# Kernel optimization log

Measured on AMD Instinct MI355X. Metric: run time of the kernel, lower is better.

The kernel has to match this reference:

```python
import jax, jax.numpy as jnp
import numpy as np
from jax import lax

NH = 4          # num_head
DIM = 512       # attention dim
VDIM = 512      # v_dim
QDIM = 1024     # q_dim
KS = 100        # loc_kernel_size -> conv width 2*KS+1
KN = 100        # loc_kernel_num
TEMP = 0.5      # temperature
BS, TS = 8, 2048


def setup_inputs() -> dict:
    key = jax.random.key(0)
    ks = jax.random.split(key, 12)
    s = 0.05
    return {
        "dec_state": jax.random.normal(ks[0], (BS, QDIM), jnp.float32),
        "enc_feat": jax.random.normal(ks[1], (BS, TS, VDIM), jnp.float32),
        "enc_len": jax.random.randint(ks[2], (BS,), TS // 2, TS + 1).astype(jnp.int32),
        "Wq": jax.random.normal(ks[3], (NH * DIM, QDIM), jnp.float32) * s,
        "bq": jnp.zeros((NH * DIM,), jnp.float32),
        "Wk": jax.random.normal(ks[4], (NH * DIM, VDIM), jnp.float32) * s,
        "bk": jnp.zeros((NH * DIM,), jnp.float32),
        "Wv": jax.random.normal(ks[5], (NH * VDIM, VDIM), jnp.float32) * s,
        "bv": jnp.zeros((NH * VDIM,), jnp.float32),
        "loc_conv_w": jax.random.normal(ks[6], (KN, NH, 2 * KS + 1), jnp.float32) * s,
        "loc_proj_w": jax.random.normal(ks[7], (DIM, KN), jnp.float32) * s,
        "gen_w": jax.random.normal(ks[8], (1, DIM), jnp.float32) * s,
        "gen_b": jnp.zeros((1,), jnp.float32),
        "merge_w": jax.random.normal(ks[9], (VDIM, NH * VDIM), jnp.float32) * s,
        "merge_b": jnp.zeros((VDIM,), jnp.float32),
    }


def reference(dec_state, enc_feat, enc_len, Wq, bq, Wk, bk, Wv, bv,
              loc_conv_w, loc_proj_w, gen_w, gen_b, merge_w, merge_b):
    bs, ts, _ = enc_feat.shape
    # query: [bs, nh, dim]
    query = jnp.tanh(dec_state @ Wq.T + bq).reshape(bs, NH, DIM)
    # key/value: [bs, nh, ts, dim]/[bs, nh, ts, v_dim]
    key = jnp.tanh(enc_feat @ Wk.T + bk).reshape(bs, ts, NH, DIM).transpose(0, 2, 1, 3)
    value = jnp.tanh(enc_feat @ Wv.T + bv).reshape(bs, ts, NH, VDIM).transpose(0, 2, 1, 3)
    # mask & initial (uniform-over-valid) previous attention
    pos = jnp.arange(ts)
    pad_mask = pos[None, :] >= enc_len[:, None]                      # [bs, ts] True = padded
    prev = jnp.where(pad_mask, 0.0, 1.0 / enc_len[:, None].astype(jnp.float32))  # [bs, ts]
    prev_att = jnp.broadcast_to(prev[:, None, :], (bs, NH, ts))      # [bs, nh, ts]
    # location features: Conv1d(nh -> kn, width 2*KS+1, pad KS, no bias)
    conv = lax.conv_general_dilated(prev_att, loc_conv_w, (1,), [(KS, KS)],
                                    dimension_numbers=("NCH", "OIH", "NCH"))  # [bs, kn, ts]
    loc = jnp.tanh(jnp.einsum("bkt,dk->btd", conv, loc_proj_w))      # [bs, ts, dim]
    # additive energy: gen_energy(tanh(k + q + loc))
    e = jnp.tanh(key + query[:, :, None, :] + loc[:, None, :, :])    # [bs, nh, ts, dim]
    energy = jnp.einsum("bhtd,d->bht", e, gen_w[0]) + gen_b[0]
    energy = energy / TEMP
    energy = jnp.where(pad_mask[:, None, :], -jnp.inf, energy)
    attn = jax.nn.softmax(energy, axis=-1)                           # [bs, nh, ts]
    ctx = jnp.einsum("bht,bhtv->bhv", attn, value).reshape(bs, NH * VDIM)
    context = ctx @ merge_w.T + merge_b                              # [bs, v_dim]
    return attn, context
```

## Files before the change

### kernel.cpp

```cpp
#include <hip/hip_runtime.h>
#include <math.h>

#define NH 4
#define DIM 512
#define VDIM 512
#define QDIM 1024
#define KS 100
#define KN 100
#define TEMPERATURE 0.5f
#define BS 8
#define TS 2048
#define NHD (NH * DIM)

#define WS_QUERY  0
#define WS_QTAB   16384
#define WS_ENERGY 119808
#define WS_CTX    185344
#define WS_P      201728
#define WS_F32_END 221928

typedef __bf16 bf16x8 __attribute__((ext_vector_type(8)));
typedef __bf16 bf16x4 __attribute__((ext_vector_type(4)));
typedef float  f32x4  __attribute__((ext_vector_type(4)));

#define AS1(p) ((const __attribute__((address_space(1))) void*)(p))
#define AS3(p) ((__attribute__((address_space(3))) void*)(p))

__device__ __forceinline__ float fast_tanh(float x) {
    float xc = fminf(fmaxf(x, -9.0f), 9.0f);
    float e = __expf(2.0f * xc);
    return __fdividef(e - 1.0f, e + 1.0f);
}

#define NE4 (BS * TS * VDIM / 4)
#define NW4 (NHD * VDIM / 4)
#define NCVT ((NE4 + 2 * NW4) / 256)
#define NQRY (BS * NHD / 4)
__global__ void k_precvt(const float* __restrict__ enc, const float* __restrict__ Wk,
                         const float* __restrict__ Wv, __bf16* __restrict__ enc_bf,
                         __bf16* __restrict__ wk_bf, __bf16* __restrict__ wv_bf,
                         const float* __restrict__ dec, const float* __restrict__ Wq,
                         const float* __restrict__ bq, float* __restrict__ query,
                         const float* __restrict__ convw, float* __restrict__ P) {
    if (blockIdx.x < NCVT) {
        int i = blockIdx.x * blockDim.x + threadIdx.x;
        const float* src; __bf16* dst; int k;
        if (i < NE4)            { src = enc; dst = enc_bf; k = i; }
        else if (i < NE4 + NW4) { src = Wk;  dst = wk_bf;  k = i - NE4; }
        else                    { src = Wv;  dst = wv_bf;  k = i - NE4 - NW4; }
        float4 v = ((const float4*)src)[k];
        bf16x4 o;
        o[0] = (__bf16)v.x; o[1] = (__bf16)v.y; o[2] = (__bf16)v.z; o[3] = (__bf16)v.w;
        ((bf16x4*)dst)[k] = o;
    } else if (blockIdx.x < NCVT + NQRY) {
        int q = blockIdx.x - NCVT;
        int w = q * 4 + (threadIdx.x >> 6);
        int lane = threadIdx.x & 63;
        int b = w >> 11;
        int o = w & 2047;
        const float* dr = dec + b * QDIM;
        const float* wr = Wq + o * QDIM;
        float s = 0.f;
        #pragma unroll
        for (int i = 0; i < QDIM / 64; ++i)
            s = fmaf(dr[lane + 64 * i], wr[lane + 64 * i], s);
        #pragma unroll
        for (int off = 32; off > 0; off >>= 1) s += __shfl_down(s, off);
        if (lane == 0) query[b * NHD + o] = tanhf(s + bq[o]);
    } else {
        int k = threadIdx.x;
        if (k < KN) {
            const float* wr = convw + k * (NH * (2 * KS + 1));
            float acc = 0.f;
            P[k] = 0.f;
            for (int dt = 0; dt < 2 * KS + 1; ++dt) {
                acc += wr[dt] + wr[201 + dt] + wr[402 + dt] + wr[603 + dt];
                P[(dt + 1) * KN + k] = acc;
            }
        }
    }
}

__global__ void k_qtab(const float* __restrict__ P, const float* __restrict__ projw,
                       float* __restrict__ Qtab) {
    int j = blockIdx.x;
    __shared__ float Pc[KN];
    int tid = threadIdx.x;
    if (tid < KN) Pc[tid] = P[j * KN + tid];
    __syncthreads();
    const float* pr = projw + tid * KN;
    float s = 0.f;
    #pragma unroll 4
    for (int k = 0; k < KN; ++k) s = fmaf(pr[k], Pc[k], s);
    Qtab[j * DIM + tid] = s;
}

#define GEMM1(Bptr)                                                               \
    const int bid = blockIdx.x;                                                    \
    const int b   = bid >> 8;                                                      \
    const int t0  = ((bid >> 4) & 15) << 7;                                        \
    const int n0  = ((((bid >> 3) & 1) << 3) | (bid & 7)) << 7;                    \
    const int len = enc_len[b];                                                    \
    if (t0 >= len) return;                                                         \
    const int tid = threadIdx.x;                                                   \
    const int w = tid >> 6, lane = tid & 63;                                       \
    const int wy = w >> 2, wx = w & 3;                                             \
    const int col = lane & 15, quad = lane >> 4;                                   \
    __shared__ __bf16 Ash[2 * 4096];                                               \
    __shared__ __bf16 Bsh[2 * 4096];                                               \
    f32x4 acc[4][2];                                                               \
    _Pragma("unroll")                                                              \
    for (int i = 0; i < 4; ++i)                                                    \
        _Pragma("unroll")                                                          \
        for (int j = 0; j < 2; ++j) acc[i][j] = (f32x4)0.f;                        \
    const __bf16* Abase = enc_bf + ((size_t)b * TS + t0) * VDIM;                   \
    const int sm = tid >> 2;                                                       \
    const int sj = (tid & 3) ^ (sm & 3) ^ ((sm >> 2) & 3);                         \
    const __bf16* gpA = Abase + (size_t)sm * VDIM + sj * 8;                        \
    const __bf16* gpB = (Bptr) + ((size_t)n0 + sm) * VDIM + sj * 8;                \
    const int cfr = quad ^ (col & 3) ^ ((col >> 2) & 3);                           \
    const char* pA = (const char*)Ash + (((wy * 64 + col) * 4 + cfr) << 4);        \
    const char* pB = (const char*)Bsh + (((wx * 32 + col) * 4 + cfr) << 4);        \
    __builtin_amdgcn_global_load_lds(AS1(gpA), AS3(Ash + w * 512), 16, 0, 0);      \
    __builtin_amdgcn_global_load_lds(AS1(gpB), AS3(Bsh + w * 512), 16, 0, 0);      \
    gpA += 32; gpB += 32;                                                          \
    for (int kk = 0; kk < 16; ++kk) {                                              \
        __syncthreads();                                                           \
        if (kk < 15) {                                                             \
            int nb_ = ((kk + 1) & 1) * 4096;                                       \
            __builtin_amdgcn_global_load_lds(AS1(gpA), AS3(Ash + nb_ + w * 512), 16, 0, 0); \
            __builtin_amdgcn_global_load_lds(AS1(gpB), AS3(Bsh + nb_ + w * 512), 16, 0, 0); \
            gpA += 32; gpB += 32;                                                  \
        }                                                                          \
        const int bo = (kk & 1) * 8192;                                            \
        bf16x8 af[4], bfr[2];                                                      \
        _Pragma("unroll")                                                          \
        for (int i = 0; i < 4; ++i) af[i] = *(const bf16x8*)(pA + bo + i * 1024);  \
        _Pragma("unroll")                                                          \
        for (int j = 0; j < 2; ++j) bfr[j] = *(const bf16x8*)(pB + bo + j * 1024); \
        _Pragma("unroll")                                                          \
        for (int i = 0; i < 4; ++i)                                                \
            _Pragma("unroll")                                                      \
            for (int j = 0; j < 2; ++j)                                            \
                acc[i][j] = __builtin_amdgcn_mfma_f32_16x16x32_bf16(               \
                    af[i], bfr[j], acc[i][j], 0, 0, 0);                            \
    }                                                                              \
    __syncthreads();

__global__ __launch_bounds__(512, 4) void k_energy(
    const __bf16* __restrict__ enc_bf, const __bf16* __restrict__ wk_bf,
    const float* __restrict__ bk, const float* __restrict__ gen_w,
    const int* __restrict__ enc_len, const float* __restrict__ query,
    const float* __restrict__ Qtab, float* __restrict__ energy) {
    GEMM1(wk_bf)

    const int h = n0 >> 9;
    const float inv_len = 1.0f / (float)len;
    float qv[2], gw[2], bkv[2], lI[2];
    int dj[2];
    #pragma unroll
    for (int j = 0; j < 2; ++j) {
        int n = n0 + wx * 32 + j * 16 + col;
        dj[j] = n & (DIM - 1);
        qv[j] = query[b * NHD + n];
        gw[j] = gen_w[dj[j]];
        bkv[j] = bk[n];
        lI[j] = fast_tanh((Qtab[(2 * KS + 1) * DIM + dj[j]] - Qtab[dj[j]]) * inv_len);
    }
    float* red = (float*)Ash;
    #pragma unroll
    for (int i = 0; i < 4; ++i) {
        #pragma unroll
        for (int r = 0; r < 4; ++r) {
            int tl = wy * 64 + i * 16 + quad * 4 + r;
            int t = t0 + tl;
            float l[2];
            if (t >= KS && t < len - KS) {
                #pragma unroll
                for (int j = 0; j < 2; ++j) l[j] = lI[j];
            } else {
                int lo = KS - t; if (lo < 0) lo = 0;
                int hi = KS - t + len - 1; if (hi > 2 * KS) hi = 2 * KS;
                bool has = (hi >= lo);
                #pragma unroll
                for (int j = 0; j < 2; ++j) {
                    float cv = has
                        ? (Qtab[(hi + 1) * DIM + dj[j]] - Qtab[lo * DIM + dj[j]]) * inv_len
                        : 0.f;
                    l[j] = fast_tanh(cv);
                }
            }
            float s = 0.f;
            #pragma unroll
            for (int j = 0; j < 2; ++j) {
                float key = fast_tanh(acc[i][j][r] + bkv[j]);
                float e = fast_tanh(key + qv[j] + l[j]);
                s = fmaf(e, gw[j], s);
            }
            s += __shfl_xor(s, 1); s += __shfl_xor(s, 2);
            s += __shfl_xor(s, 4); s += __shfl_xor(s, 8);
            if (col == 0) red[tl * 4 + wx] = s;
        }
    }
    __syncthreads();
    if (tid < 128) {
        float s = red[tid * 4] + red[tid * 4 + 1] + red[tid * 4 + 2] + red[tid * 4 + 3];
        atomicAdd(&energy[(size_t)(b * NH + h) * TS + t0 + tid], s);
    }
}

__global__ __launch_bounds__(512, 4) void k_ctxg(
    const __bf16* __restrict__ enc_bf, const __bf16* __restrict__ wv_bf,
    const float* __restrict__ bv, const float* __restrict__ attn,
    const int* __restrict__ enc_len, float* __restrict__ ctx) {
    GEMM1(wv_bf)

    const int h = n0 >> 9;
    float att[4][4];
    #pragma unroll
    for (int i = 0; i < 4; ++i)
        #pragma unroll
        for (int r = 0; r < 4; ++r)
            att[i][r] = attn[(size_t)(b * NH + h) * TS + t0 + wy * 64 + i * 16 + quad * 4 + r];
    float* red = (float*)Ash;
    #pragma unroll
    for (int j = 0; j < 2; ++j) {
        int nl = wx * 32 + j * 16 + col;
        float bvn = bv[n0 + nl];
        float s = 0.f;
        #pragma unroll
        for (int i = 0; i < 4; ++i)
            #pragma unroll
            for (int r = 0; r < 4; ++r)
                s = fmaf(att[i][r], fast_tanh(acc[i][j][r] + bvn), s);
        s += __shfl_xor(s, 16); s += __shfl_xor(s, 32);
        if (quad == 0) red[nl * 2 + wy] = s;
    }
    __syncthreads();
    if (tid < 128) {
        float s = red[tid * 2] + red[tid * 2 + 1];
        atomicAdd(&ctx[(size_t)b * NHD + n0 + tid], s);
    }
}

__global__ void k_softmax(const float* __restrict__ energy, const int* __restrict__ enc_len,
                          const float* __restrict__ gen_b, float* __restrict__ attn) {
    int bh = blockIdx.x;
    int b = bh >> 2;
    int len = enc_len[b];
    int tid = threadIdx.x;
    int w = tid >> 6, lane = tid & 63;
    const float gb = gen_b[0];
    float ev[4];
    float mx = -INFINITY;
    #pragma unroll
    for (int i = 0; i < 4; ++i) {
        int t = i * 512 + tid;
        float e = (t < len) ? (energy[(size_t)bh * TS + t] + gb) * (1.0f / TEMPERATURE)
                            : -INFINITY;
        ev[i] = e;
        mx = fmaxf(mx, e);
    }
    __shared__ float sred[8], ssum[8];
    #pragma unroll
    for (int off = 32; off > 0; off >>= 1) mx = fmaxf(mx, __shfl_xor(mx, off));
    if (lane == 0) sred[w] = mx;
    __syncthreads();
    #pragma unroll
    for (int k = 0; k < 8; ++k) mx = fmaxf(mx, sred[k]);
    float ls = 0.f;
    #pragma unroll
    for (int i = 0; i < 4; ++i) {
        float ex = __expf(ev[i] - mx);
        ev[i] = ex;
        ls += ex;
    }
    #pragma unroll
    for (int off = 32; off > 0; off >>= 1) ls += __shfl_xor(ls, off);
    if (lane == 0) ssum[w] = ls;
    __syncthreads();
    float tot = 0.f;
    #pragma unroll
    for (int k = 0; k < 8; ++k) tot += ssum[k];
    float inv = 1.0f / tot;
    #pragma unroll
    for (int i = 0; i < 4; ++i)
        attn[(size_t)bh * TS + i * 512 + tid] = ev[i] * inv;
}

__global__ void k_merge(const float* __restrict__ ctx, const float* __restrict__ mw,
                        const float* __restrict__ mb, float* __restrict__ out) {
    int w = (blockIdx.x * blockDim.x + threadIdx.x) >> 6;
    int lane = threadIdx.x & 63;
    int b = w >> 9;
    int o = w & 511;
    const float* c = ctx + (size_t)b * NHD;
    const float* wr = mw + (size_t)o * NHD;
    float s = 0.f;
    #pragma unroll
    for (int i = 0; i < NHD / 64; ++i) s = fmaf(c[lane + 64 * i], wr[lane + 64 * i], s);
    #pragma unroll
    for (int off = 32; off > 0; off >>= 1) s += __shfl_down(s, off);
    if (lane == 0) out[b * VDIM + o] = s + mb[o];
}

extern "C" void kernel_launch(void* const* d_in, const int* in_sizes, int n_in,
                              void* d_out, int out_size, void* d_ws, size_t ws_size,
                              hipStream_t stream) {
    const float* dec     = (const float*)d_in[0];
    const float* enc     = (const float*)d_in[1];
    const int*   enc_len = (const int*)d_in[2];
    const float* Wq      = (const float*)d_in[3];
    const float* bq      = (const float*)d_in[4];
    const float* Wk      = (const float*)d_in[5];
    const float* bk      = (const float*)d_in[6];
    const float* Wv      = (const float*)d_in[7];
    const float* bv      = (const float*)d_in[8];
    const float* convw   = (const float*)d_in[9];
    const float* projw   = (const float*)d_in[10];
    const float* gen_w   = (const float*)d_in[11];
    const float* gen_b   = (const float*)d_in[12];
    const float* merge_w = (const float*)d_in[13];
    const float* merge_b = (const float*)d_in[14];

    float* out   = (float*)d_out;
    float* ws    = (float*)d_ws;
    float* query = ws + WS_QUERY;
    float* Qtab  = ws + WS_QTAB;
    float* energy= ws + WS_ENERGY;
    float* ctx   = ws + WS_CTX;
    float* Pws   = ws + WS_P;
    __bf16* enc_bf = (__bf16*)((char*)d_ws + (size_t)WS_F32_END * 4);
    __bf16* wk_bf  = enc_bf + (size_t)BS * TS * VDIM;
    __bf16* wv_bf  = wk_bf + (size_t)NHD * VDIM;

    hipMemsetAsync(energy, 0, (65536 + 16384) * sizeof(float), stream);

    k_precvt<<<dim3(NCVT + NQRY + 1), dim3(256), 0, stream>>>(
        enc, Wk, Wv, enc_bf, wk_bf, wv_bf, dec, Wq, bq, query, convw, Pws);
    k_qtab<<<dim3(2 * KS + 2), dim3(512), 0, stream>>>(Pws, projw, Qtab);
    k_energy<<<dim3(2048), dim3(512), 0, stream>>>(
        enc_bf, wk_bf, bk, gen_w, enc_len, query, Qtab, energy);
    k_softmax<<<dim3(BS * NH), dim3(512), 0, stream>>>(energy, enc_len, gen_b, out);
    k_ctxg<<<dim3(2048), dim3(512), 0, stream>>>(
        enc_bf, wv_bf, bv, out, enc_len, ctx);
    k_merge<<<dim3(BS * VDIM / 4), dim3(256), 0, stream>>>(ctx, merge_w, merge_b, out + 65536);
}
```

Baseline: 330.5 us.

## Widen GEMM tiles to 128x256 with 1024-thread blocks and split conv prefix kernel

The shared key/value GEMM macro now uses 1024-thread blocks that each compute a 128x256 output tile. Every loaded encoder tile is therefore reused across twice as many weight columns, and the grid is halved. The reduction layouts in the energy and context kernels are adjusted to the 8-wide wave split. The serial conv-weight prefix-sum tail block moves out of the conversion kernel into its own kernel, which stages the per-channel sums in LDS in parallel before the scan. In exchange this adds an extra launch, doubles LDS for B, and the launch bound of (1024, 4) may squeeze registers and cause spills.

```diff
diff --git a/kernel.cpp b/kernel.cpp
--- a/kernel.cpp
+++ b/kernel.cpp
@@ -40,8 +40,7 @@
                          const float* __restrict__ Wv, __bf16* __restrict__ enc_bf,
                          __bf16* __restrict__ wk_bf, __bf16* __restrict__ wv_bf,
                          const float* __restrict__ dec, const float* __restrict__ Wq,
-                         const float* __restrict__ bq, float* __restrict__ query,
-                         const float* __restrict__ convw, float* __restrict__ P) {
+                         const float* __restrict__ bq, float* __restrict__ query) {
     if (blockIdx.x < NCVT) {
         int i = blockIdx.x * blockDim.x + threadIdx.x;
         const float* src; __bf16* dst; int k;
@@ -52,7 +51,7 @@
         bf16x4 o;
         o[0] = (__bf16)v.x; o[1] = (__bf16)v.y; o[2] = (__bf16)v.z; o[3] = (__bf16)v.w;
         ((bf16x4*)dst)[k] = o;
-    } else if (blockIdx.x < NCVT + NQRY) {
+    } else {
         int q = blockIdx.x - NCVT;
         int w = q * 4 + (threadIdx.x >> 6);
         int lane = threadIdx.x & 63;
@@ -67,16 +66,26 @@
         #pragma unroll
         for (int off = 32; off > 0; off >>= 1) s += __shfl_down(s, off);
         if (lane == 0) query[b * NHD + o] = tanhf(s + bq[o]);
-    } else {
-        int k = threadIdx.x;
-        if (k < KN) {
-            const float* wr = convw + k * (NH * (2 * KS + 1));
-            float acc = 0.f;
-            P[k] = 0.f;
-            for (int dt = 0; dt < 2 * KS + 1; ++dt) {
-                acc += wr[dt] + wr[201 + dt] + wr[402 + dt] + wr[603 + dt];
-                P[(dt + 1) * KN + k] = acc;
-            }
+    }
+}
+
+__global__ void k_prefix(const float* __restrict__ convw, float* __restrict__ P) {
+    __shared__ float cs[KN * (2 * KS + 1)];
+    int tid = threadIdx.x;
+    for (int i = tid; i < KN * (2 * KS + 1); i += 1024) {
+        int k = i / (2 * KS + 1);
+        int dt = i - k * (2 * KS + 1);
+        const float* wr = convw + k * (NH * (2 * KS + 1)) + dt;
+        cs[i] = wr[0] + wr[201] + wr[402] + wr[603];
+    }
+    __syncthreads();
+    if (tid < KN) {
+        float acc = 0.f;
+        P[tid] = 0.f;
+        const float* c = cs + tid * (2 * KS + 1);
+        for (int dt = 0; dt < 2 * KS + 1; ++dt) {
+            acc += c[dt];
+            P[(dt + 1) * KN + tid] = acc;
         }
     }
 }
@@ -97,47 +106,54 @@
 
 #define GEMM1(Bptr)                                                               \
     const int bid = blockIdx.x;                                                    \
-    const int b   = bid >> 8;                                                      \
-    const int t0  = ((bid >> 4) & 15) << 7;                                        \
-    const int n0  = ((((bid >> 3) & 1) << 3) | (bid & 7)) << 7;                    \
+    const int b   = bid >> 7;                                                      \
+    const int t0  = ((bid >> 3) & 15) << 7;                                        \
+    const int n0  = (bid & 7) << 8;                                                \
     const int len = enc_len[b];                                                    \
     if (t0 >= len) return;                                                         \
     const int tid = threadIdx.x;                                                   \
     const int w = tid >> 6, lane = tid & 63;                                       \
-    const int wy = w >> 2, wx = w & 3;                                             \
+    const int wy = w >> 3, wx = w & 7;                                             \
     const int col = lane & 15, quad = lane >> 4;                                   \
     __shared__ __bf16 Ash[2 * 4096];                                               \
-    __shared__ __bf16 Bsh[2 * 4096];                                               \
+    __shared__ __bf16 Bsh[2 * 8192];                                               \
     f32x4 acc[4][2];                                                               \
     _Pragma("unroll")                                                              \
     for (int i = 0; i < 4; ++i)                                                    \
         _Pragma("unroll")                                                          \
         for (int j = 0; j < 2; ++j) acc[i][j] = (f32x4)0.f;                        \
     const __bf16* Abase = enc_bf + ((size_t)b * TS + t0) * VDIM;                   \
-    const int sm = tid >> 2;                                                       \
-    const int sj = (tid & 3) ^ (sm & 3) ^ ((sm >> 2) & 3);                         \
-    const __bf16* gpA = Abase + (size_t)sm * VDIM + sj * 8;                        \
-    const __bf16* gpB = (Bptr) + ((size_t)n0 + sm) * VDIM + sj * 8;                \
+    const int mB_ = tid >> 2;                                                      \
+    const int cB_ = (tid & 3) ^ (mB_ & 3) ^ ((mB_ >> 2) & 3);                      \
+    const __bf16* gpB = (Bptr) + ((size_t)n0 + mB_) * VDIM + cB_ * 8;              \
+    const int mA_ = (tid & 511) >> 2;                                              \
+    const int cA_ = (tid & 3) ^ (mA_ & 3) ^ ((mA_ >> 2) & 3);                      \
+    const __bf16* gpA = Abase + (size_t)mA_ * VDIM + cA_ * 8;                      \
     const int cfr = quad ^ (col & 3) ^ ((col >> 2) & 3);                           \
     const char* pA = (const char*)Ash + (((wy * 64 + col) * 4 + cfr) << 4);        \
     const char* pB = (const char*)Bsh + (((wx * 32 + col) * 4 + cfr) << 4);        \
-    __builtin_amdgcn_global_load_lds(AS1(gpA), AS3(Ash + w * 512), 16, 0, 0);      \
-    __builtin_amdgcn_global_load_lds(AS1(gpB), AS3(Bsh + w * 512), 16, 0, 0);      \
+    if (tid < 512)                                                                 \
+        __builtin_amdgcn_global_load_lds(AS1(gpA), AS3(Ash + tid * 8), 16, 0, 0);  \
+    __builtin_amdgcn_global_load_lds(AS1(gpB), AS3(Bsh + tid * 8), 16, 0, 0);      \
     gpA += 32; gpB += 32;                                                          \
     for (int kk = 0; kk < 16; ++kk) {                                              \
         __syncthreads();                                                           \
         if (kk < 15) {                                                             \
-            int nb_ = ((kk + 1) & 1) * 4096;                                       \
-            __builtin_amdgcn_global_load_lds(AS1(gpA), AS3(Ash + nb_ + w * 512), 16, 0, 0); \
-            __builtin_amdgcn_global_load_lds(AS1(gpB), AS3(Bsh + nb_ + w * 512), 16, 0, 0); \
+            const int par = (kk + 1) & 1;                                          \
+            if (tid < 512)                                                         \
+                __builtin_amdgcn_global_load_lds(AS1(gpA),                         \
+                    AS3(Ash + par * 4096 + tid * 8), 16, 0, 0);                    \
+            __builtin_amdgcn_global_load_lds(AS1(gpB),                             \
+                AS3(Bsh + par * 8192 + tid * 8), 16, 0, 0);                        \
             gpA += 32; gpB += 32;                                                  \
         }                                                                          \
-        const int bo = (kk & 1) * 8192;                                            \
+        const int boA = (kk & 1) * 8192;                                           \
+        const int boB = (kk & 1) * 16384;                                          \
         bf16x8 af[4], bfr[2];                                                      \
         _Pragma("unroll")                                                          \
-        for (int i = 0; i < 4; ++i) af[i] = *(const bf16x8*)(pA + bo + i * 1024);  \
+        for (int i = 0; i < 4; ++i) af[i] = *(const bf16x8*)(pA + boA + i * 1024); \
         _Pragma("unroll")                                                          \
-        for (int j = 0; j < 2; ++j) bfr[j] = *(const bf16x8*)(pB + bo + j * 1024); \
+        for (int j = 0; j < 2; ++j) bfr[j] = *(const bf16x8*)(pB + boB + j * 1024);\
         _Pragma("unroll")                                                          \
         for (int i = 0; i < 4; ++i)                                                \
             _Pragma("unroll")                                                      \
@@ -147,7 +163,7 @@
     }                                                                              \
     __syncthreads();
 
-__global__ __launch_bounds__(512, 4) void k_energy(
+__global__ __launch_bounds__(1024, 4) void k_energy(
     const __bf16* __restrict__ enc_bf, const __bf16* __restrict__ wk_bf,
     const float* __restrict__ bk, const float* __restrict__ gen_w,
     const int* __restrict__ enc_len, const float* __restrict__ query,
@@ -199,17 +215,19 @@
             }
             s += __shfl_xor(s, 1); s += __shfl_xor(s, 2);
             s += __shfl_xor(s, 4); s += __shfl_xor(s, 8);
-            if (col == 0) red[tl * 4 + wx] = s;
+            if (col == 0) red[tl * 8 + wx] = s;
         }
     }
     __syncthreads();
     if (tid < 128) {
-        float s = red[tid * 4] + red[tid * 4 + 1] + red[tid * 4 + 2] + red[tid * 4 + 3];
+        float s = 0.f;
+        #pragma unroll
+        for (int x = 0; x < 8; ++x) s += red[tid * 8 + x];
         atomicAdd(&energy[(size_t)(b * NH + h) * TS + t0 + tid], s);
     }
 }
 
-__global__ __launch_bounds__(512, 4) void k_ctxg(
+__global__ __launch_bounds__(1024, 4) void k_ctxg(
     const __bf16* __restrict__ enc_bf, const __bf16* __restrict__ wv_bf,
     const float* __restrict__ bv, const float* __restrict__ attn,
     const int* __restrict__ enc_len, float* __restrict__ ctx) {
@@ -237,7 +255,7 @@
         if (quad == 0) red[nl * 2 + wy] = s;
     }
     __syncthreads();
-    if (tid < 128) {
+    if (tid < 256) {
         float s = red[tid * 2] + red[tid * 2 + 1];
         atomicAdd(&ctx[(size_t)b * NHD + n0 + tid], s);
     }
@@ -336,13 +354,14 @@
 
     hipMemsetAsync(energy, 0, (65536 + 16384) * sizeof(float), stream);
 
-    k_precvt<<<dim3(NCVT + NQRY + 1), dim3(256), 0, stream>>>(
-        enc, Wk, Wv, enc_bf, wk_bf, wv_bf, dec, Wq, bq, query, convw, Pws);
+    k_prefix<<<dim3(1), dim3(1024), 0, stream>>>(convw, Pws);
+    k_precvt<<<dim3(NCVT + NQRY), dim3(256), 0, stream>>>(
+        enc, Wk, Wv, enc_bf, wk_bf, wv_bf, dec, Wq, bq, query);
     k_qtab<<<dim3(2 * KS + 2), dim3(512), 0, stream>>>(Pws, projw, Qtab);
-    k_energy<<<dim3(2048), dim3(512), 0, stream>>>(
+    k_energy<<<dim3(1024), dim3(1024), 0, stream>>>(
         enc_bf, wk_bf, bk, gen_w, enc_len, query, Qtab, energy);
     k_softmax<<<dim3(BS * NH), dim3(512), 0, stream>>>(energy, enc_len, gen_b, out);
-    k_ctxg<<<dim3(2048), dim3(512), 0, stream>>>(
+    k_ctxg<<<dim3(1024), dim3(1024), 0, stream>>>(
         enc_bf, wv_bf, bv, out, enc_len, ctx);
     k_merge<<<dim3(BS * VDIM / 4), dim3(256), 0, stream>>>(ctx, merge_w, merge_b, out + 65536);
 }
```

After: 351.6 us. 1.06x slower.
